# Kernel tuning notes

Measured on AMD Instinct MI355X. Metric: run time of the kernel, lower is better.

The kernel has to match this reference:

```python
import jax, jax.numpy as jnp
import numpy as np

TEMPERATURE = 0.07
EPS = 1e-12  # matches F.normalize eps clamp


def setup_inputs() -> dict:
    key = jax.random.key(0)
    k1, k2 = jax.random.split(key)
    B, S, D = 8, 512, 128
    return {
        "z_i": jax.random.normal(k1, (B, S, D), dtype=jnp.float32),
        "z_j": jax.random.normal(k2, (B, S, D), dtype=jnp.float32),
    }


def reference(z_i, z_j):
    D = z_i.shape[-1]
    zi = z_i.reshape(-1, D)  # [N, D]
    zj = z_j.reshape(-1, D)
    # cosine normalization (use_cosine_similarity=True)
    zi = zi / jnp.maximum(jnp.linalg.norm(zi, axis=1, keepdims=True), EPS)
    zj = zj / jnp.maximum(jnp.linalg.norm(zj, axis=1, keepdims=True), EPS)
    N = zi.shape[0]
    z = jnp.concatenate([zi, zj], axis=0)  # [2N, D]
    sim = (z @ z.T) / TEMPERATURE  # [2N, 2N]
    # denominator: logsumexp over all j != i (positives + negatives)
    diag = jnp.eye(2 * N, dtype=bool)
    lse = jax.nn.logsumexp(jnp.where(diag, -jnp.inf, sim), axis=1)  # [2N]
    # positive logit for row i is sim[i, (i+N) mod 2N] = <zi, zj>/T for both halves
    pos_half = jnp.sum(zi * zj, axis=1) / TEMPERATURE  # [N]
    pos = jnp.concatenate([pos_half, pos_half])  # [2N]
    return jnp.mean(-pos + lse)
```

## Files before the change

kernel.cpp:

```cpp
#include <hip/hip_runtime.h>
#include <stdint.h>


#define TOTAL   8192
#define NHALF   4096
#define DK      128
#define TEMP_INV 14.285714285714286f
#define SCALE    4.539816f

#define TILE    128
#define TILES   (TOTAL / TILE)
#define NBLK    (TILES * (TILES + 1) / 2)

typedef short  bf16x8  __attribute__((ext_vector_type(8)));
typedef float  floatx4 __attribute__((ext_vector_type(4)));

#if __has_builtin(__builtin_amdgcn_exp2f)
#define EXP2(x) __builtin_amdgcn_exp2f(x)
#else
#define EXP2(x) exp2f(x)
#endif

__device__ __forceinline__ uint32_t f2bf(float f) {
  uint32_t u = __float_as_uint(f);
  return (u + 0x7fffu + ((u >> 16) & 1u)) >> 16;
}
__device__ __forceinline__ uint32_t pack2bf(float lo, float hi) {
  return f2bf(lo) | (f2bf(hi) << 16);
}

__global__ __launch_bounds__(256) void ntx_norm(
    const float* __restrict__ zi, const float* __restrict__ zj,
    uint32_t* __restrict__ zn,
    float* __restrict__ pos)
{
  const int t = threadIdx.x;
  const int wave = t >> 6, lane = t & 63;
  const int i = blockIdx.x * 4 + wave;

  const float2 vi = *(const float2*)(zi + (size_t)i * DK + lane * 2);
  const float2 vj = *(const float2*)(zj + (size_t)i * DK + lane * 2);
  float ssi = vi.x * vi.x + vi.y * vi.y;
  float ssj = vj.x * vj.x + vj.y * vj.y;
  float dij = vi.x * vj.x + vi.y * vj.y;
#pragma unroll
  for (int m = 1; m <= 32; m <<= 1) {
    ssi += __shfl_xor(ssi, m, 64);
    ssj += __shfl_xor(ssj, m, 64);
    dij += __shfl_xor(dij, m, 64);
  }
  const float invi = 1.0f / fmaxf(sqrtf(ssi), 1e-12f);
  const float invj = 1.0f / fmaxf(sqrtf(ssj), 1e-12f);

  zn[(size_t)i * 64 + lane] =
      pack2bf(vi.x * invi * SCALE, vi.y * invi * SCALE);
  zn[(size_t)(i + NHALF) * 64 + lane] =
      pack2bf(vj.x * invj * SCALE, vj.y * invj * SCALE);
  if (lane == 0) pos[i] = dij * invi * invj * TEMP_INV;
}

__global__ __launch_bounds__(256) void ntx_gemm(
    const uint16_t* __restrict__ z,
    float* __restrict__ scratch)
{
  __shared__ float rowacc[4][64];
  __shared__ float colacc[4][64];

  int I = 0, rem = (int)blockIdx.x, span = TILES;
  while (rem >= span) { rem -= span; --span; ++I; }
  const int J = I + rem;
  const bool isdiag = (I == J);

  const int t = threadIdx.x;
  const int w = t >> 6, lane = t & 63;
  const int q = lane >> 4, c = lane & 15;
  const int rowbase = I * TILE + (w >> 1) * 64;
  const int colbase = J * TILE + (w & 1) * 64;

  bf16x8 afrag[4][4];
  bf16x8 bfrag[4][4];
#pragma unroll
  for (int s = 0; s < 4; ++s) {
    const uint16_t* ap = z + (size_t)(rowbase + s * 16 + c) * DK + q * 8;
    const uint16_t* bp = z + (size_t)(colbase + s * 16 + c) * DK + q * 8;
#pragma unroll
    for (int kk = 0; kk < 4; ++kk) {
      afrag[s][kk] = *(const bf16x8*)(ap + kk * 32);
      bfrag[s][kk] = *(const bf16x8*)(bp + kk * 32);
    }
  }

  float runsum[4][4];
#pragma unroll
  for (int s = 0; s < 4; ++s)
#pragma unroll
    for (int r = 0; r < 4; ++r) runsum[s][r] = 0.0f;

#pragma unroll
  for (int jt = 0; jt < 4; ++jt) {
    const int jc = colbase + jt * 16;
    float colv = 0.0f;
#pragma unroll
    for (int s = 0; s < 4; ++s) {
      floatx4 acc = {0.0f, 0.0f, 0.0f, 0.0f};
#pragma unroll
      for (int kk = 0; kk < 4; ++kk)
        acc = __builtin_amdgcn_mfma_f32_16x16x32_bf16(afrag[s][kk],
                                                      bfrag[jt][kk], acc,
                                                      0, 0, 0);
      const int rb = rowbase + s * 16;
      if (!isdiag) {
#pragma unroll
        for (int r = 0; r < 4; ++r) {
          float e = EXP2(acc[r]);
          runsum[s][r] += e;
          colv += e;
        }
      } else if (jc == rb) {
#pragma unroll
        for (int r = 0; r < 4; ++r) {
          float e = EXP2(acc[r]);
          runsum[s][r] += (q * 4 + r == c) ? 0.0f : e;
        }
      } else {
#pragma unroll
        for (int r = 0; r < 4; ++r) runsum[s][r] += EXP2(acc[r]);
      }
    }

    if (!isdiag) {
      colv += __shfl_xor(colv, 16, 64);
      colv += __shfl_xor(colv, 32, 64);
      if (lane < 16)
        colacc[w][jt * 16 + lane] = colv;
    }
  }

#pragma unroll
  for (int s = 0; s < 4; ++s)
#pragma unroll
    for (int r = 0; r < 4; ++r) {
      float v = runsum[s][r];
      v += __shfl_xor(v, 1, 64);
      v += __shfl_xor(v, 2, 64);
      v += __shfl_xor(v, 4, 64);
      v += __shfl_xor(v, 8, 64);
      runsum[s][r] = v;
    }
  if (c == 0) {
#pragma unroll
    for (int s = 0; s < 4; ++s)
#pragma unroll
      for (int r = 0; r < 4; ++r)
        rowacc[w][s * 16 + q * 4 + r] = runsum[s][r];
  }

  __syncthreads();
  float* sblk = scratch + (size_t)blockIdx.x * 256;
  if (t < TILE) {
    const int h = t >> 6, o = t & 63;
    sblk[t] = rowacc[2 * h][o] + rowacc[2 * h + 1][o];
    if (!isdiag)
      sblk[128 + t] = colacc[h][o] + colacc[h + 2][o];
  }
}

__global__ __launch_bounds__(256) void ntx_redu(
    const float* __restrict__ scratch, float* __restrict__ lpart)
{
  __shared__ float sbuf[128];
  __shared__ float red[2];

  const int I = (int)blockIdx.x;
  const int o = (int)threadIdx.x & 127;
  const int half = (int)threadIdx.x >> 7;

  float S = 0.0f;
  if (half == 0) {
    int id = I * TILES - (I * (I - 1)) / 2;
#pragma unroll 8
    for (int Jt = I; Jt < TILES; ++Jt, ++id)
      S += scratch[(size_t)id * 256 + o];
  } else {
    int idc = I;
#pragma unroll 8
    for (int Ip = 0; Ip < I; ++Ip) {
      S += scratch[(size_t)idc * 256 + 128 + o];
      idc += TILES - 1 - Ip;
    }
  }
  if (half) sbuf[o] = S;
  __syncthreads();
  if (!half) {
    float v = __logf(S + sbuf[o]);
#pragma unroll
    for (int m = 1; m <= 32; m <<= 1) v += __shfl_xor(v, m, 64);
    if ((o & 63) == 0) red[o >> 6] = v;
  }
  __syncthreads();
  if (threadIdx.x == 0) lpart[I] = red[0] + red[1];
}

__global__ __launch_bounds__(256) void ntx_final(
    const float* __restrict__ lpart, const float* __restrict__ pos,
    float* __restrict__ out)
{
  const int t = threadIdx.x;
  float acc = (t < TILES) ? lpart[t] : 0.0f;
  for (int r = t; r < NHALF; r += 256) acc -= 2.0f * pos[r];
#pragma unroll
  for (int m = 1; m <= 32; m <<= 1) acc += __shfl_xor(acc, m, 64);
  __shared__ float red[4];
  if ((t & 63) == 0) red[t >> 6] = acc;
  __syncthreads();
  if (t == 0) out[0] = (red[0] + red[1] + red[2] + red[3]) / (float)TOTAL;
}

extern "C" void kernel_launch(void* const* d_in, const int* in_sizes, int n_in,
                              void* d_out, int out_size, void* d_ws,
                              size_t ws_size, hipStream_t stream) {
  const float* zi = (const float*)d_in[0];
  const float* zj = (const float*)d_in[1];
  float* out = (float*)d_out;

  char* ws = (char*)d_ws;
  uint16_t* zn      = (uint16_t*)ws;
  float*    scratch = (float*)(ws + (size_t)TOTAL * DK * 2);
  float*    lpart   = (float*)(ws + (size_t)TOTAL * DK * 2
                               + (size_t)NBLK * 256 * 4);
  float*    pos     = (float*)(ws + (size_t)TOTAL * DK * 2
                               + (size_t)NBLK * 256 * 4 + 256);

  ntx_norm<<<dim3(NHALF / 4), dim3(256), 0, stream>>>(zi, zj, (uint32_t*)zn,
                                                      pos);
  ntx_gemm<<<dim3(NBLK), dim3(256), 0, stream>>>(zn, scratch);
  ntx_redu<<<dim3(TILES), dim3(256), 0, stream>>>(scratch, lpart);
  ntx_final<<<dim3(1), dim3(256), 0, stream>>>(lpart, pos, out);
}
```

Baseline: 105.8 us.

## Process up to four column tiles per block with double-buffered B fragments

Each GEMM block now keeps its A row-tile fragments in registers and walks up to four column tiles of the upper triangle. It double-buffers the B fragment loads so the next tile's global loads overlap the current tile's MFMA and exp work. This cuts the block count from 2080 to 544 and reuses A loads across several tiles. The shared-memory reduction is replaced by direct per-wave partial writes, and the reduce kernel is reworked to index the new layout. The risks are higher register pressure, since launch_bounds asks for 2 blocks per SIMD, and fewer blocks to balance load across CUs.

```diff
diff --git a/kernel.cpp b/kernel.cpp
--- a/kernel.cpp
+++ b/kernel.cpp
@@ -10,7 +10,8 @@
 
 #define TILE    128
 #define TILES   (TOTAL / TILE)
-#define NBLK    (TILES * (TILES + 1) / 2)
+#define NJ      4
+#define NBLK2   544
 
 typedef short  bf16x8  __attribute__((ext_vector_type(8)));
 typedef float  floatx4 __attribute__((ext_vector_type(4)));
@@ -59,35 +60,29 @@
   if (lane == 0) pos[i] = dij * invi * invj * TEMP_INV;
 }
 
-__global__ __launch_bounds__(256) void ntx_gemm(
+__global__ __launch_bounds__(256, 2) void ntx_gemm(
     const uint16_t* __restrict__ z,
-    float* __restrict__ scratch)
-{
-  __shared__ float rowacc[4][64];
-  __shared__ float colacc[4][64];
-
-  int I = 0, rem = (int)blockIdx.x, span = TILES;
-  while (rem >= span) { rem -= span; --span; ++I; }
-  const int J = I + rem;
-  const bool isdiag = (I == J);
+    float* __restrict__ rowpart,
+    float* __restrict__ colpart)
+{
+  int b = (int)blockIdx.x, I = 0;
+  for (;;) { const int G = (67 - I) >> 2; if (b < G) break; b -= G; ++I; }
+  const int Jbase = I + 4 * b;
+  const int nt = (TILES - Jbase) < NJ ? (TILES - Jbase) : NJ;
 
   const int t = threadIdx.x;
   const int w = t >> 6, lane = t & 63;
   const int q = lane >> 4, c = lane & 15;
-  const int rowbase = I * TILE + (w >> 1) * 64;
-  const int colbase = J * TILE + (w & 1) * 64;
+  const int rhalf = w >> 1, chalf = w & 1;
+  const int rowbase = I * TILE + rhalf * 64;
 
   bf16x8 afrag[4][4];
-  bf16x8 bfrag[4][4];
 #pragma unroll
   for (int s = 0; s < 4; ++s) {
     const uint16_t* ap = z + (size_t)(rowbase + s * 16 + c) * DK + q * 8;
-    const uint16_t* bp = z + (size_t)(colbase + s * 16 + c) * DK + q * 8;
-#pragma unroll
-    for (int kk = 0; kk < 4; ++kk) {
+#pragma unroll
+    for (int kk = 0; kk < 4; ++kk)
       afrag[s][kk] = *(const bf16x8*)(ap + kk * 32);
-      bfrag[s][kk] = *(const bf16x8*)(bp + kk * 32);
-    }
   }
 
   float runsum[4][4];
@@ -96,43 +91,71 @@
 #pragma unroll
     for (int r = 0; r < 4; ++r) runsum[s][r] = 0.0f;
 
-#pragma unroll
-  for (int jt = 0; jt < 4; ++jt) {
-    const int jc = colbase + jt * 16;
-    float colv = 0.0f;
+  auto LOADB = [&](int Jt, bf16x8 (&dst)[4][4]) {
+    const int colb = Jt * TILE + chalf * 64;
 #pragma unroll
     for (int s = 0; s < 4; ++s) {
-      floatx4 acc = {0.0f, 0.0f, 0.0f, 0.0f};
+      const uint16_t* bp = z + (size_t)(colb + s * 16 + c) * DK + q * 8;
 #pragma unroll
       for (int kk = 0; kk < 4; ++kk)
-        acc = __builtin_amdgcn_mfma_f32_16x16x32_bf16(afrag[s][kk],
-                                                      bfrag[jt][kk], acc,
-                                                      0, 0, 0);
-      const int rb = rowbase + s * 16;
+        dst[s][kk] = *(const bf16x8*)(bp + kk * 32);
+    }
+  };
+
+  auto COMP = [&](int Jt, int jslot, const bf16x8 (&bb)[4][4]) {
+    const int colbase = Jt * TILE + chalf * 64;
+    const bool isdiag = (Jt == I);
+#pragma unroll
+    for (int jt = 0; jt < 4; ++jt) {
+      const int jc = colbase + jt * 16;
+      float colv = 0.0f;
+#pragma unroll
+      for (int s = 0; s < 4; ++s) {
+        floatx4 acc = {0.0f, 0.0f, 0.0f, 0.0f};
+#pragma unroll
+        for (int kk = 0; kk < 4; ++kk)
+          acc = __builtin_amdgcn_mfma_f32_16x16x32_bf16(afrag[s][kk],
+                                                        bb[jt][kk], acc,
+                                                        0, 0, 0);
+        const int rb = rowbase + s * 16;
+        if (isdiag && jc == rb) {
+#pragma unroll
+          for (int r = 0; r < 4; ++r) {
+            float e = EXP2(acc[r]);
+            runsum[s][r] += (q * 4 + r == c) ? 0.0f : e;
+          }
+        } else {
+#pragma unroll
+          for (int r = 0; r < 4; ++r) {
+            float e = EXP2(acc[r]);
+            runsum[s][r] += e;
+            colv += e;
+          }
+        }
+      }
       if (!isdiag) {
-#pragma unroll
-        for (int r = 0; r < 4; ++r) {
-          float e = EXP2(acc[r]);
-          runsum[s][r] += e;
-          colv += e;
+        colv += __shfl_xor(colv, 16, 64);
+        colv += __shfl_xor(colv, 32, 64);
+        if (lane < 16) {
+          float* cp = colpart +
+              ((((size_t)blockIdx.x * NJ + jslot) * 2 + chalf) * 2 + rhalf) * 64;
+          cp[jt * 16 + lane] = colv;
         }
-      } else if (jc == rb) {
-#pragma unroll
-        for (int r = 0; r < 4; ++r) {
-          float e = EXP2(acc[r]);
-          runsum[s][r] += (q * 4 + r == c) ? 0.0f : e;
-        }
-      } else {
-#pragma unroll
-        for (int r = 0; r < 4; ++r) runsum[s][r] += EXP2(acc[r]);
       }
     }
-
-    if (!isdiag) {
-      colv += __shfl_xor(colv, 16, 64);
-      colv += __shfl_xor(colv, 32, 64);
-      if (lane < 16)
-        colacc[w][jt * 16 + lane] = colv;
+  };
+
+  bf16x8 b0[4][4], b1[4][4];
+  LOADB(Jbase, b0);
+  if (nt > 1) LOADB(Jbase + 1, b1);
+  COMP(Jbase, 0, b0);
+  if (nt > 1) {
+    if (nt > 2) LOADB(Jbase + 2, b0);
+    COMP(Jbase + 1, 1, b1);
+    if (nt > 2) {
+      if (nt > 3) LOADB(Jbase + 3, b1);
+      COMP(Jbase + 2, 2, b0);
+      if (nt > 3) COMP(Jbase + 3, 3, b1);
     }
   }
 
@@ -148,45 +171,46 @@
       runsum[s][r] = v;
     }
   if (c == 0) {
+    float* rp = rowpart + ((size_t)blockIdx.x * 2 + chalf) * 128 + rhalf * 64;
 #pragma unroll
     for (int s = 0; s < 4; ++s)
 #pragma unroll
       for (int r = 0; r < 4; ++r)
-        rowacc[w][s * 16 + q * 4 + r] = runsum[s][r];
-  }
-
-  __syncthreads();
-  float* sblk = scratch + (size_t)blockIdx.x * 256;
-  if (t < TILE) {
-    const int h = t >> 6, o = t & 63;
-    sblk[t] = rowacc[2 * h][o] + rowacc[2 * h + 1][o];
-    if (!isdiag)
-      sblk[128 + t] = colacc[h][o] + colacc[h + 2][o];
+        rp[s * 16 + q * 4 + r] = runsum[s][r];
   }
 }
 
 __global__ __launch_bounds__(256) void ntx_redu(
-    const float* __restrict__ scratch, float* __restrict__ lpart)
+    const float* __restrict__ rowpart, const float* __restrict__ colpart,
+    float* __restrict__ lpart)
 {
   __shared__ float sbuf[128];
   __shared__ float red[2];
 
   const int I = (int)blockIdx.x;
-  const int o = (int)threadIdx.x & 127;
-  const int half = (int)threadIdx.x >> 7;
+  const int t = (int)threadIdx.x;
+  const int o = t & 127;
+  const int half = t >> 7;
 
   float S = 0.0f;
   if (half == 0) {
-    int id = I * TILES - (I * (I - 1)) / 2;
-#pragma unroll 8
-    for (int Jt = I; Jt < TILES; ++Jt, ++id)
-      S += scratch[(size_t)id * 256 + o];
+    int bS = 0;
+    for (int Ip = 0; Ip < I; ++Ip) bS += (67 - Ip) >> 2;
+    const int G = (67 - I) >> 2;
+    for (int gg = 0; gg < G; ++gg) {
+      const float* rp = rowpart + (size_t)(bS + gg) * 2 * 128;
+      S += rp[o] + rp[128 + o];
+    }
   } else {
-    int idc = I;
-#pragma unroll 8
+    const int h = o >> 6, l = o & 63;
+    int bS = 0;
     for (int Ip = 0; Ip < I; ++Ip) {
-      S += scratch[(size_t)idc * 256 + 128 + o];
-      idc += TILES - 1 - Ip;
+      const int d = I - Ip;
+      const int bid = bS + (d >> 2);
+      const int jj = d & 3;
+      const float* cp = colpart + (((size_t)bid * NJ + jj) * 2 + h) * 2 * 64;
+      S += cp[l] + cp[64 + l];
+      bS += (67 - Ip) >> 2;
     }
   }
   if (half) sbuf[o] = S;
@@ -198,7 +222,7 @@
     if ((o & 63) == 0) red[o >> 6] = v;
   }
   __syncthreads();
-  if (threadIdx.x == 0) lpart[I] = red[0] + red[1];
+  if (t == 0) lpart[I] = red[0] + red[1];
 }
 
 __global__ __launch_bounds__(256) void ntx_final(
@@ -224,16 +248,19 @@
   float* out = (float*)d_out;
 
   char* ws = (char*)d_ws;
-  uint16_t* zn      = (uint16_t*)ws;
-  float*    scratch = (float*)(ws + (size_t)TOTAL * DK * 2);
-  float*    lpart   = (float*)(ws + (size_t)TOTAL * DK * 2
-                               + (size_t)NBLK * 256 * 4);
-  float*    pos     = (float*)(ws + (size_t)TOTAL * DK * 2
-                               + (size_t)NBLK * 256 * 4 + 256);
+  uint16_t* zn = (uint16_t*)ws;
+  size_t off = (size_t)TOTAL * DK * 2;
+  float* rowpart = (float*)(ws + off);
+  off += (size_t)NBLK2 * 2 * 128 * 4;
+  float* colpart = (float*)(ws + off);
+  off += (size_t)NBLK2 * NJ * 2 * 2 * 64 * 4;
+  float* lpart = (float*)(ws + off);
+  off += 256 * 4;
+  float* pos = (float*)(ws + off);
 
   ntx_norm<<<dim3(NHALF / 4), dim3(256), 0, stream>>>(zi, zj, (uint32_t*)zn,
                                                       pos);
-  ntx_gemm<<<dim3(NBLK), dim3(256), 0, stream>>>(zn, scratch);
-  ntx_redu<<<dim3(TILES), dim3(256), 0, stream>>>(scratch, lpart);
+  ntx_gemm<<<dim3(NBLK2), dim3(256), 0, stream>>>(zn, rowpart, colpart);
+  ntx_redu<<<dim3(TILES), dim3(256), 0, stream>>>(rowpart, colpart, lpart);
   ntx_final<<<dim3(1), dim3(256), 0, stream>>>(lpart, pos, out);
 }
```

Result: slower. 130.1 us (+23.0%).

## Stage B tile in padded LDS and split GEMM tile across eight waves

Applied to the files above, without the earlier changes.

The GEMM block now uses 512 threads (8 waves), each owning a 16-row strip of the 128x128 tile instead of a 64x64 quadrant. The B (column) tile is loaded once into padded shared memory and read by all waves, rather than each wave loading its own fragments from global memory into registers. The intent is to cut per-thread register pressure (from 32 bf16x8 fragments down to 4 A plus 4 transient B) so occupancy rises, and to reduce redundant global loads. In exchange it adds an LDS staging pass and a barrier, and column sums now accumulate over eight waves.

```diff
diff --git a/kernel.cpp b/kernel.cpp
--- a/kernel.cpp
+++ b/kernel.cpp
@@ -11,6 +11,7 @@
 #define TILE    128
 #define TILES   (TOTAL / TILE)
 #define NBLK    (TILES * (TILES + 1) / 2)
+#define WAVES   8
 
 typedef short  bf16x8  __attribute__((ext_vector_type(8)));
 typedef float  floatx4 __attribute__((ext_vector_type(4)));
@@ -59,12 +60,12 @@
   if (lane == 0) pos[i] = dij * invi * invj * TEMP_INV;
 }
 
-__global__ __launch_bounds__(256) void ntx_gemm(
+__global__ __launch_bounds__(512, 8) void ntx_gemm(
     const uint16_t* __restrict__ z,
     float* __restrict__ scratch)
 {
-  __shared__ float rowacc[4][64];
-  __shared__ float colacc[4][64];
+  __shared__ uint4 lb4[TILE * 17];
+  __shared__ float colacc[WAVES][TILE];
 
   int I = 0, rem = (int)blockIdx.x, span = TILES;
   while (rem >= span) { rem -= span; --span; ++I; }
@@ -74,94 +75,82 @@
   const int t = threadIdx.x;
   const int w = t >> 6, lane = t & 63;
   const int q = lane >> 4, c = lane & 15;
-  const int rowbase = I * TILE + (w >> 1) * 64;
-  const int colbase = J * TILE + (w & 1) * 64;
-
-  bf16x8 afrag[4][4];
-  bf16x8 bfrag[4][4];
-#pragma unroll
-  for (int s = 0; s < 4; ++s) {
-    const uint16_t* ap = z + (size_t)(rowbase + s * 16 + c) * DK + q * 8;
-    const uint16_t* bp = z + (size_t)(colbase + s * 16 + c) * DK + q * 8;
-#pragma unroll
-    for (int kk = 0; kk < 4; ++kk) {
-      afrag[s][kk] = *(const bf16x8*)(ap + kk * 32);
-      bfrag[s][kk] = *(const bf16x8*)(bp + kk * 32);
+  const int i0 = I * TILE;
+  const int j0 = J * TILE;
+  const int rowbase = i0 + w * 16;
+
+  bf16x8 afrag[4];
+  {
+    const uint16_t* ap = z + (size_t)(rowbase + c) * DK + q * 8;
+#pragma unroll
+    for (int kk = 0; kk < 4; ++kk)
+      afrag[kk] = *(const bf16x8*)(ap + kk * 32);
+  }
+
+  {
+    const int r0 = t >> 4, ch = t & 15;
+#pragma unroll
+    for (int p = 0; p < 4; ++p) {
+      const int r = r0 + p * 32;
+      lb4[r * 17 + ch] = *(const uint4*)(z + (size_t)(j0 + r) * DK + ch * 8);
     }
   }
-
-  float runsum[4][4];
-#pragma unroll
-  for (int s = 0; s < 4; ++s)
-#pragma unroll
-    for (int r = 0; r < 4; ++r) runsum[s][r] = 0.0f;
-
-#pragma unroll
-  for (int jt = 0; jt < 4; ++jt) {
-    const int jc = colbase + jt * 16;
-    float colv = 0.0f;
-#pragma unroll
-    for (int s = 0; s < 4; ++s) {
-      floatx4 acc = {0.0f, 0.0f, 0.0f, 0.0f};
-#pragma unroll
-      for (int kk = 0; kk < 4; ++kk)
-        acc = __builtin_amdgcn_mfma_f32_16x16x32_bf16(afrag[s][kk],
-                                                      bfrag[jt][kk], acc,
-                                                      0, 0, 0);
-      const int rb = rowbase + s * 16;
+  __syncthreads();
+
+  float runsum[4] = {0.0f, 0.0f, 0.0f, 0.0f};
+
+#pragma unroll
+  for (int jt = 0; jt < TILE / 16; ++jt) {
+    const int jc = j0 + jt * 16;
+    bf16x8 bfrag[4];
+#pragma unroll
+    for (int kk = 0; kk < 4; ++kk)
+      bfrag[kk] = *(const bf16x8*)&lb4[(jt * 16 + c) * 17 + kk * 4 + q];
+
+    floatx4 acc = {0.0f, 0.0f, 0.0f, 0.0f};
+#pragma unroll
+    for (int kk = 0; kk < 4; ++kk)
+      acc = __builtin_amdgcn_mfma_f32_16x16x32_bf16(afrag[kk], bfrag[kk],
+                                                    acc, 0, 0, 0);
+    if (isdiag && jc == rowbase) {
+#pragma unroll
+      for (int r = 0; r < 4; ++r) {
+        float e = EXP2(acc[r]);
+        runsum[r] += (q * 4 + r == c) ? 0.0f : e;
+      }
+    } else {
+      float colv = 0.0f;
+#pragma unroll
+      for (int r = 0; r < 4; ++r) {
+        float e = EXP2(acc[r]);
+        runsum[r] += e;
+        colv += e;
+      }
       if (!isdiag) {
-#pragma unroll
-        for (int r = 0; r < 4; ++r) {
-          float e = EXP2(acc[r]);
-          runsum[s][r] += e;
-          colv += e;
-        }
-      } else if (jc == rb) {
-#pragma unroll
-        for (int r = 0; r < 4; ++r) {
-          float e = EXP2(acc[r]);
-          runsum[s][r] += (q * 4 + r == c) ? 0.0f : e;
-        }
-      } else {
-#pragma unroll
-        for (int r = 0; r < 4; ++r) runsum[s][r] += EXP2(acc[r]);
+        colv += __shfl_xor(colv, 16, 64);
+        colv += __shfl_xor(colv, 32, 64);
+        if (lane < 16) colacc[w][jt * 16 + lane] = colv;
       }
     }
-
-    if (!isdiag) {
-      colv += __shfl_xor(colv, 16, 64);
-      colv += __shfl_xor(colv, 32, 64);
-      if (lane < 16)
-        colacc[w][jt * 16 + lane] = colv;
-    }
-  }
-
-#pragma unroll
-  for (int s = 0; s < 4; ++s)
-#pragma unroll
-    for (int r = 0; r < 4; ++r) {
-      float v = runsum[s][r];
-      v += __shfl_xor(v, 1, 64);
-      v += __shfl_xor(v, 2, 64);
-      v += __shfl_xor(v, 4, 64);
-      v += __shfl_xor(v, 8, 64);
-      runsum[s][r] = v;
-    }
-  if (c == 0) {
-#pragma unroll
-    for (int s = 0; s < 4; ++s)
-#pragma unroll
-      for (int r = 0; r < 4; ++r)
-        rowacc[w][s * 16 + q * 4 + r] = runsum[s][r];
-  }
-
-  __syncthreads();
+  }
+
   float* sblk = scratch + (size_t)blockIdx.x * 256;
-  if (t < TILE) {
-    const int h = t >> 6, o = t & 63;
-    sblk[t] = rowacc[2 * h][o] + rowacc[2 * h + 1][o];
-    if (!isdiag)
-      sblk[128 + t] = colacc[h][o] + colacc[h + 2][o];
+#pragma unroll
+  for (int r = 0; r < 4; ++r) {
+    float v = runsum[r];
+    v += __shfl_xor(v, 1, 64);
+    v += __shfl_xor(v, 2, 64);
+    v += __shfl_xor(v, 4, 64);
+    v += __shfl_xor(v, 8, 64);
+    if (c == 0) sblk[w * 16 + q * 4 + r] = v;
+  }
+
+  __syncthreads();
+  if (!isdiag && t < TILE) {
+    float s = 0.0f;
+#pragma unroll
+    for (int ww = 0; ww < WAVES; ++ww) s += colacc[ww][t];
+    sblk[128 + t] = s;
   }
 }
 
@@ -233,7 +222,7 @@
 
   ntx_norm<<<dim3(NHALF / 4), dim3(256), 0, stream>>>(zi, zj, (uint32_t*)zn,
                                                       pos);
-  ntx_gemm<<<dim3(NBLK), dim3(256), 0, stream>>>(zn, scratch);
+  ntx_gemm<<<dim3(NBLK), dim3(512), 0, stream>>>(zn, scratch);
   ntx_redu<<<dim3(TILES), dim3(256), 0, stream>>>(scratch, lpart);
   ntx_final<<<dim3(1), dim3(256), 0, stream>>>(lpart, pos, out);
 }
```

Result: faster. 90.41 us (-14.5%).
